# Performance work log

Hardware: AMD Instinct MI355X
Metric: run time of the kernel (lower is better)

## Reference

```python
import jax, jax.numpy as jnp
import numpy as np

B, S, E, U, V = 64, 1024, 1024, 1024, 32000

def setup_inputs() -> dict:
    key = jax.random.key(0)
    ks = jax.random.split(key, 12)
    s = lambda fan_in: 1.0 / np.sqrt(fan_in)
    return {
        "sentence": jax.random.randint(ks[0], (B, S), 0, V, dtype=jnp.int64),
        "emb": jax.random.normal(ks[1], (V, E), jnp.float32),
        "Wf": jax.random.normal(ks[2], (E, U), jnp.float32) * s(E),
        "bf": jnp.zeros((U,), jnp.float32),
        "Wi": jax.random.normal(ks[3], (E, U), jnp.float32) * s(E),
        "bi": jnp.zeros((U,), jnp.float32),
        "Wh": jax.random.normal(ks[4], (E, U), jnp.float32) * s(E),
        "bh": jnp.zeros((U,), jnp.float32),
        "W1": jax.random.normal(ks[5], (U, 64), jnp.float32) * s(U),
        "b1": jnp.zeros((64,), jnp.float32),
        "W2": jax.random.normal(ks[6], (64, 1), jnp.float32) * s(64),
        "b2": jnp.zeros((1,), jnp.float32),
    }

def reference(sentence, emb, Wf, bf, Wi, bi, Wh, bh, W1, b1, W2, b2):
    x = emb[sentence]                                   # [B,S,E]
    # minLSTM gates depend only on x -> hoist GEMMs out of the time loop
    f = jax.nn.sigmoid(jnp.einsum('bse,eu->bsu', x, Wf) + bf)
    i = jax.nn.sigmoid(jnp.einsum('bse,eu->bsu', x, Wi) + bi)
    h_tilde = jnp.einsum('bse,eu->bsu', x, Wh) + bh
    denom = f + i
    f_n = f / denom                                     # normalized forget gate
    i_n = i / denom                                     # normalized input gate

    def step(h, gates):
        f_t, ih_t = gates                               # [B,U] each
        h = f_t * h + ih_t
        return h, None

    h0 = jnp.zeros((sentence.shape[0], Wf.shape[1]), x.dtype)
    # scan over time; precombine i_n * h_tilde
    gates = (jnp.swapaxes(f_n, 0, 1), jnp.swapaxes(i_n * h_tilde, 0, 1))  # [S,B,U]
    h, _ = jax.lax.scan(step, h0, gates)
    z = h @ W1 + b1
    z = z @ W2 + b2
    return jax.nn.sigmoid(z)                            # [B,1]
```

## Files before the change

kernel.cpp:

```cpp
#include <hip/hip_runtime.h>
#include <cstdint>

typedef unsigned short u16;
typedef __attribute__((ext_vector_type(8))) short short8;
typedef __attribute__((ext_vector_type(8))) unsigned short ushort8;
typedef __attribute__((ext_vector_type(4))) float floatx4;
typedef __attribute__((ext_vector_type(8))) _Float16 half8;

#define S_LEN 1024
#define BATCH 64
#define EDIM 1024
#define UDIM 1024
#define VOCAB 32000
#define NTOT (3 * UDIM)
#define CT 64
#define NC (S_LEN / CT)
#define BUFE (128 * 64 + 192 * 64)

__device__ __forceinline__ u16 f2bf(float x) {
  unsigned u = __float_as_uint(x);
  return (u16)((u + 0x7fffu + ((u >> 16) & 1u)) >> 16);
}

__device__ __forceinline__ void async16(const u16* g, u16* s) {
  __builtin_amdgcn_global_load_lds(
      (__attribute__((address_space(1))) void*)(uintptr_t)g,
      (__attribute__((address_space(3))) void*)(uintptr_t)s,
      16, 0, 0);
}

__device__ __forceinline__ float sigm(float x) {
  return __builtin_amdgcn_rcpf(1.f + __expf(-x));
}

__global__ __launch_bounds__(256) void conv_emb(const float4* __restrict__ in,
                                                ushort4* __restrict__ out, int n4) {
  const int stride = gridDim.x * 256;
  for (int i = blockIdx.x * 256 + threadIdx.x; i < n4; i += stride) {
    float4 v = in[i];
    ushort4 o;
    o.x = f2bf(v.x); o.y = f2bf(v.y); o.z = f2bf(v.z); o.w = f2bf(v.w);
    out[i] = o;
  }
}

__global__ __launch_bounds__(256) void conv_wt(const float* __restrict__ Wf,
                                               const float* __restrict__ Wi,
                                               const float* __restrict__ Wh,
                                               u16* __restrict__ wtB) {
  __shared__ float t[32][33];
  const float* W = (blockIdx.z == 0) ? Wf : ((blockIdx.z == 1) ? Wi : Wh);
  int bx = blockIdx.x * 32;
  int by = blockIdx.y * 32;
  int tx = threadIdx.x, ty = threadIdx.y;
  for (int j = 0; j < 32; j += 8)
    t[ty + j][tx] = W[(size_t)(by + ty + j) * UDIM + bx + tx];
  __syncthreads();
  u16* out = wtB + (size_t)blockIdx.z * UDIM * EDIM;
  for (int j = 0; j < 32; j += 8)
    out[(size_t)(bx + ty + j) * EDIM + by + tx] = f2bf(t[tx][ty + j]);
}

__global__ __launch_bounds__(256, 2) void gate_gemm(
    const u16* __restrict__ embB, const u16* __restrict__ wtB,
    const float* __restrict__ bfp, const float* __restrict__ bip,
    const float* __restrict__ bhp, u16* __restrict__ FG) {
  __shared__ __align__(16) u16 SM[2 * BUFE];

  const int tid = threadIdx.x;
  const int wave = tid >> 6;
  const int lane = tid & 63;

  const int g = blockIdx.x;
  const int x = g & 7;
  const int s = g >> 3;
  const int mtile = s >> 1;
  const int utile = x * 2 + (s & 1);
  const int m0 = mtile * 128;
  const int u0 = utile * 64;

  const u16* gA[4]; int loA[4];
  const u16* gB[6]; int loB[6];
#pragma unroll
  for (int j = 0; j < 4; ++j) {
    int idx = j * 256 + tid;
    int r = idx >> 3;
    int cg = (idx & 7) ^ (r & 7);
    gA[j] = embB + (size_t)(m0 + r) * EDIM + cg * 8;
    loA[j] = idx * 8;
  }
#pragma unroll
  for (int j = 0; j < 6; ++j) {
    int idx = j * 256 + tid;
    int r = idx >> 3;
    int gr = (r >> 6) * UDIM + u0 + (r & 63);
    int cg = (idx & 7) ^ (r & 7);
    gB[j] = wtB + (size_t)gr * EDIM + cg * 8;
    loB[j] = 128 * 64 + idx * 8;
  }

  floatx4 acc[8][3] = {};
  const int fr = lane & 15;
  const int fq = lane >> 4;
  const int fr7 = fr & 7;
  const int un = wave * 16 + fr;

#pragma unroll
  for (int j = 0; j < 4; ++j) async16(gA[j], &SM[loA[j]]);
#pragma unroll
  for (int j = 0; j < 6; ++j) async16(gB[j], &SM[loB[j]]);
  asm volatile("s_waitcnt vmcnt(0)" ::: "memory");
  __builtin_amdgcn_s_barrier();
  __builtin_amdgcn_sched_barrier(0);

  int cur = 0;
  for (int t = 0; t < EDIM / 64; ++t) {
    if (t + 1 < EDIM / 64) {
      const int k0 = (t + 1) * 64;
      u16* nb = SM + (cur ^ 1) * BUFE;
#pragma unroll
      for (int j = 0; j < 4; ++j) async16(gA[j] + k0, &nb[loA[j]]);
#pragma unroll
      for (int j = 0; j < 6; ++j) async16(gB[j] + k0, &nb[loB[j]]);
    }
    __builtin_amdgcn_sched_barrier(0);
    const u16* As = SM + cur * BUFE;
    const u16* Bs = As + 128 * 64;
#pragma unroll
    for (int kk = 0; kk < 2; ++kk) {
      const int swz = ((kk * 4 + fq) ^ fr7) * 8;
      short8 b0 = *(const short8*)&Bs[(0 * 64 + un) * 64 + swz];
      short8 b1 = *(const short8*)&Bs[(1 * 64 + un) * 64 + swz];
      short8 b2 = *(const short8*)&Bs[(2 * 64 + un) * 64 + swz];
#pragma unroll
      for (int mt = 0; mt < 8; ++mt) {
        short8 am = *(const short8*)&As[(mt * 16 + fr) * 64 + swz];
        acc[mt][0] = __builtin_amdgcn_mfma_f32_16x16x32_bf16(am, b0, acc[mt][0], 0, 0, 0);
        acc[mt][1] = __builtin_amdgcn_mfma_f32_16x16x32_bf16(am, b1, acc[mt][1], 0, 0, 0);
        acc[mt][2] = __builtin_amdgcn_mfma_f32_16x16x32_bf16(am, b2, acc[mt][2], 0, 0, 0);
      }
    }
    __builtin_amdgcn_sched_barrier(0);
    asm volatile("s_waitcnt vmcnt(0)" ::: "memory");
    __builtin_amdgcn_s_barrier();
    __builtin_amdgcn_sched_barrier(0);
    cur ^= 1;
  }

  const int ug = u0 + un;
  const float bfv = bfp[ug], biv = bip[ug], bhv = bhp[ug];
  u16* FGs = SM;
  const int up = un ^ ((fq & 1) << 4);
#pragma unroll
  for (int mt = 0; mt < 8; ++mt) {
#pragma unroll
    for (int r = 0; r < 4; ++r) {
      float fs = sigm(acc[mt][0][r] + bfv);
      float is = sigm(acc[mt][1][r] + biv);
      float hv = acc[mt][2][r] + bhv;
      float inv = __builtin_amdgcn_rcpf(fs + is);
      float fn = fs * inv;
      float gv = is * inv * hv;
      int row = mt * 16 + fq * 4 + r;
      unsigned pkfg = (unsigned)__builtin_bit_cast(u16, (_Float16)fn) |
                      ((unsigned)__builtin_bit_cast(u16, (_Float16)gv) << 16);
      *(unsigned*)&FGs[row * 128 + up * 2] = pkfg;
    }
  }
  __syncthreads();
#pragma unroll
  for (int j = 0; j < 8; ++j) {
    int idx = j * 256 + tid;
    int row = idx >> 4, cc = idx & 15;
    int ccp = cc ^ (((row >> 2) & 1) << 2);
    *(ushort8*)&FG[(size_t)(m0 + row) * (2 * UDIM) + u0 * 2 + cc * 8] =
        *(const ushort8*)&FGs[row * 128 + ccp * 8];
  }
}

__global__ __launch_bounds__(256) void scan_gather(
    const int* __restrict__ sent, const u16* __restrict__ FG,
    float* __restrict__ Fc, float* __restrict__ Gc) {
  const int b = blockIdx.x >> 4;
  const int c = blockIdx.x & (NC - 1);
  const int tid = threadIdx.x;
  __shared__ int toks[CT];
  if (tid < CT) toks[tid] = sent[b * S_LEN + c * CT + tid];
  __syncthreads();
  const int uo2 = tid * 8;
  floatx4 F = {1.f, 1.f, 1.f, 1.f};
  floatx4 G = {0.f, 0.f, 0.f, 0.f};
#pragma unroll 8
  for (int t = 0; t < CT; ++t) {
    const size_t ro = (size_t)toks[t] * (2 * UDIM) + uo2;
    half8 fg = __builtin_bit_cast(half8, *(const ushort8*)&FG[ro]);
    floatx4 fn = {(float)fg[0], (float)fg[2], (float)fg[4], (float)fg[6]};
    floatx4 gv = {(float)fg[1], (float)fg[3], (float)fg[5], (float)fg[7]};
    G = fn * G + gv;
    F = F * fn;
  }
  const size_t o = (size_t)c * (BATCH * UDIM) + (size_t)b * UDIM + tid * 4;
  *(floatx4*)&Fc[o] = F;
  *(floatx4*)&Gc[o] = G;
}

__global__ __launch_bounds__(256) void mlp_head(
    const float* __restrict__ Fc, const float* __restrict__ Gc,
    const float* __restrict__ W1, const float* __restrict__ b1,
    const float* __restrict__ W2, const float* __restrict__ b2,
    float* __restrict__ out) {
  const int b = blockIdx.x;
  const int tid = threadIdx.x;
  __shared__ float h_s[UDIM];
  __shared__ float z1[64];
  for (int u = tid; u < UDIM; u += 256) {
    float h = 0.f;
#pragma unroll
    for (int c = 0; c < NC; ++c) {
      float F = Fc[c * (BATCH * UDIM) + b * UDIM + u];
      float G = Gc[c * (BATCH * UDIM) + b * UDIM + u];
      h = F * h + G;
    }
    h_s[u] = h;
  }
  __syncthreads();
  const int j = tid >> 2, p = tid & 3;
  float partial = 0.f;
  for (int u = p * 256; u < p * 256 + 256; ++u) partial += h_s[u] * W1[u * 64 + j];
  partial += __shfl_down(partial, 1);
  partial += __shfl_down(partial, 2);
  if (p == 0) z1[j] = partial + b1[j];
  __syncthreads();
  if (tid < 64) {
    float v = z1[tid] * W2[tid];
#pragma unroll
    for (int off = 32; off > 0; off >>= 1) v += __shfl_down(v, off);
    if (tid == 0) out[b] = 1.f / (1.f + __expf(-(v + b2[0])));
  }
}

extern "C" void kernel_launch(void* const* d_in, const int* in_sizes, int n_in,
                              void* d_out, int out_size, void* d_ws, size_t ws_size,
                              hipStream_t stream) {
  const int* sent = (const int*)d_in[0];
  const float* emb = (const float*)d_in[1];
  const float* Wf = (const float*)d_in[2];
  const float* bf_ = (const float*)d_in[3];
  const float* Wi = (const float*)d_in[4];
  const float* bi_ = (const float*)d_in[5];
  const float* Wh = (const float*)d_in[6];
  const float* bh_ = (const float*)d_in[7];
  const float* W1 = (const float*)d_in[8];
  const float* b1 = (const float*)d_in[9];
  const float* W2 = (const float*)d_in[10];
  const float* b2 = (const float*)d_in[11];
  float* out = (float*)d_out;

  char* ws = (char*)d_ws;
  u16* embB = (u16*)ws;   ws += (size_t)VOCAB * EDIM * 2;
  u16* wtB = (u16*)ws;    ws += (size_t)NTOT * EDIM * 2;
  u16* FG = (u16*)ws;     ws += (size_t)VOCAB * UDIM * 2 * 2;
  float* Fc = (float*)ws; ws += (size_t)NC * BATCH * UDIM * 4;
  float* Gc = (float*)ws; ws += (size_t)NC * BATCH * UDIM * 4;

  int n4 = (int)((size_t)VOCAB * EDIM / 4);
  hipLaunchKernelGGL(conv_emb, dim3(2048), dim3(256), 0, stream,
                     (const float4*)emb, (ushort4*)embB, n4);
  hipLaunchKernelGGL(conv_wt, dim3(32, 32, 3), dim3(32, 8), 0, stream, Wf, Wi, Wh, wtB);
  hipLaunchKernelGGL(gate_gemm, dim3((VOCAB / 128) * (NTOT / 192)), dim3(256), 0, stream,
                     embB, wtB, bf_, bi_, bh_, FG);
  hipLaunchKernelGGL(scan_gather, dim3(BATCH * NC), dim3(256), 0, stream,
                     sent, FG, Fc, Gc);
  hipLaunchKernelGGL(mlp_head, dim3(BATCH), dim3(256), 0, stream, Fc, Gc, W1, b1, W2, b2, out);
}
```

Before: 468.9 us.

## Restructure gate GEMM into finer-grained K-slice pipeline with higher occupancy

After: 477.5 us. No clear change (+1.8%).

```diff
diff --git a/kernel.cpp b/kernel.cpp
--- a/kernel.cpp
+++ b/kernel.cpp
@@ -15,7 +15,9 @@
 #define NTOT (3 * UDIM)
 #define CT 64
 #define NC (S_LEN / CT)
-#define BUFE (128 * 64 + 192 * 64)
+#define A_HALF 4096
+#define B_BASE 8192
+#define B_HALF 6144
 
 __device__ __forceinline__ u16 f2bf(float x) {
   unsigned u = __float_as_uint(x);
@@ -36,7 +38,17 @@
 __global__ __launch_bounds__(256) void conv_emb(const float4* __restrict__ in,
                                                 ushort4* __restrict__ out, int n4) {
   const int stride = gridDim.x * 256;
-  for (int i = blockIdx.x * 256 + threadIdx.x; i < n4; i += stride) {
+  int i = blockIdx.x * 256 + threadIdx.x;
+  for (; i + stride < n4; i += 2 * stride) {
+    float4 v0 = in[i];
+    float4 v1 = in[i + stride];
+    ushort4 o0, o1;
+    o0.x = f2bf(v0.x); o0.y = f2bf(v0.y); o0.z = f2bf(v0.z); o0.w = f2bf(v0.w);
+    o1.x = f2bf(v1.x); o1.y = f2bf(v1.y); o1.z = f2bf(v1.z); o1.w = f2bf(v1.w);
+    out[i] = o0;
+    out[i + stride] = o1;
+  }
+  if (i < n4) {
     float4 v = in[i];
     ushort4 o;
     o.x = f2bf(v.x); o.y = f2bf(v.y); o.z = f2bf(v.z); o.w = f2bf(v.w);
@@ -61,11 +73,11 @@
     out[(size_t)(bx + ty + j) * EDIM + by + tx] = f2bf(t[tx][ty + j]);
 }
 
-__global__ __launch_bounds__(256, 2) void gate_gemm(
+__global__ __launch_bounds__(256, 3) void gate_gemm(
     const u16* __restrict__ embB, const u16* __restrict__ wtB,
     const float* __restrict__ bfp, const float* __restrict__ bip,
     const float* __restrict__ bhp, u16* __restrict__ FG) {
-  __shared__ __align__(16) u16 SM[2 * BUFE];
+  __shared__ __align__(16) u16 SM[2 * A_HALF + 2 * B_HALF];
 
   const int tid = threadIdx.x;
   const int wave = tid >> 6;
@@ -79,73 +91,93 @@
   const int m0 = mtile * 128;
   const int u0 = utile * 64;
 
-  const u16* gA[4]; int loA[4];
-  const u16* gB[6]; int loB[6];
-#pragma unroll
-  for (int j = 0; j < 4; ++j) {
+  const u16* gA[2]; int loA[2];
+  const u16* gB[3]; int loB[3];
+#pragma unroll
+  for (int j = 0; j < 2; ++j) {
     int idx = j * 256 + tid;
-    int r = idx >> 3;
-    int cg = (idx & 7) ^ (r & 7);
-    gA[j] = embB + (size_t)(m0 + r) * EDIM + cg * 8;
+    int r = idx >> 2;
+    int sub = (idx & 3) ^ ((r >> 1) & 3);
+    gA[j] = embB + (size_t)(m0 + r) * EDIM + sub * 8;
     loA[j] = idx * 8;
   }
 #pragma unroll
-  for (int j = 0; j < 6; ++j) {
+  for (int j = 0; j < 3; ++j) {
     int idx = j * 256 + tid;
-    int r = idx >> 3;
+    int r = idx >> 2;
     int gr = (r >> 6) * UDIM + u0 + (r & 63);
-    int cg = (idx & 7) ^ (r & 7);
-    gB[j] = wtB + (size_t)gr * EDIM + cg * 8;
-    loB[j] = 128 * 64 + idx * 8;
+    int sub = (idx & 3) ^ ((r >> 1) & 3);
+    gB[j] = wtB + (size_t)gr * EDIM + sub * 8;
+    loB[j] = idx * 8;
   }
 
   floatx4 acc[8][3] = {};
   const int fr = lane & 15;
   const int fq = lane >> 4;
-  const int fr7 = fr & 7;
   const int un = wave * 16 + fr;
-
-#pragma unroll
-  for (int j = 0; j < 4; ++j) async16(gA[j], &SM[loA[j]]);
-#pragma unroll
-  for (int j = 0; j < 6; ++j) async16(gB[j], &SM[loB[j]]);
+  const int crd = (fq ^ ((fr >> 1) & 3)) * 8;
+
+#define STAGE(p, h)                                                  \
+  do {                                                               \
+    const int kb_ = (p) * 32;                                        \
+    _Pragma("unroll") for (int j = 0; j < 2; ++j)                    \
+        async16(gA[j] + kb_, &SM[(h) * A_HALF + loA[j]]);            \
+    _Pragma("unroll") for (int j = 0; j < 3; ++j)                    \
+        async16(gB[j] + kb_, &SM[B_BASE + (h) * B_HALF + loB[j]]);   \
+  } while (0)
+
+#define COMPUTE(h)                                                   \
+  do {                                                               \
+    const u16* Ah = SM + (h) * A_HALF;                               \
+    const u16* Bh = SM + B_BASE + (h) * B_HALF;                      \
+    short8 b0 = *(const short8*)&Bh[(0 * 64 + un) * 32 + crd];       \
+    short8 b1 = *(const short8*)&Bh[(1 * 64 + un) * 32 + crd];       \
+    short8 b2 = *(const short8*)&Bh[(2 * 64 + un) * 32 + crd];       \
+    __builtin_amdgcn_s_setprio(1);                                   \
+    _Pragma("unroll") for (int mt = 0; mt < 8; ++mt) {               \
+      short8 am = *(const short8*)&Ah[(mt * 16 + fr) * 32 + crd];    \
+      acc[mt][0] = __builtin_amdgcn_mfma_f32_16x16x32_bf16(am, b0, acc[mt][0], 0, 0, 0); \
+      acc[mt][1] = __builtin_amdgcn_mfma_f32_16x16x32_bf16(am, b1, acc[mt][1], 0, 0, 0); \
+      acc[mt][2] = __builtin_amdgcn_mfma_f32_16x16x32_bf16(am, b2, acc[mt][2], 0, 0, 0); \
+    }                                                                \
+    __builtin_amdgcn_s_setprio(0);                                   \
+  } while (0)
+
+  STAGE(0, 0);
+  STAGE(1, 1);
+  __builtin_amdgcn_sched_barrier(0);
+
+  for (int t = 0; t < 15; ++t) {
+    asm volatile("s_waitcnt vmcnt(5)" ::: "memory");
+    __builtin_amdgcn_s_barrier();
+    __builtin_amdgcn_sched_barrier(0);
+    COMPUTE(0);
+    __builtin_amdgcn_sched_barrier(0);
+    __builtin_amdgcn_s_barrier();
+    STAGE(2 * t + 2, 0);
+    __builtin_amdgcn_sched_barrier(0);
+    asm volatile("s_waitcnt vmcnt(5)" ::: "memory");
+    __builtin_amdgcn_s_barrier();
+    __builtin_amdgcn_sched_barrier(0);
+    COMPUTE(1);
+    __builtin_amdgcn_sched_barrier(0);
+    __builtin_amdgcn_s_barrier();
+    STAGE(2 * t + 3, 1);
+    __builtin_amdgcn_sched_barrier(0);
+  }
+  asm volatile("s_waitcnt vmcnt(5)" ::: "memory");
+  __builtin_amdgcn_s_barrier();
+  __builtin_amdgcn_sched_barrier(0);
+  COMPUTE(0);
+  __builtin_amdgcn_sched_barrier(0);
+  __builtin_amdgcn_s_barrier();
   asm volatile("s_waitcnt vmcnt(0)" ::: "memory");
   __builtin_amdgcn_s_barrier();
   __builtin_amdgcn_sched_barrier(0);
-
-  int cur = 0;
-  for (int t = 0; t < EDIM / 64; ++t) {
-    if (t + 1 < EDIM / 64) {
-      const int k0 = (t + 1) * 64;
-      u16* nb = SM + (cur ^ 1) * BUFE;
-#pragma unroll
-      for (int j = 0; j < 4; ++j) async16(gA[j] + k0, &nb[loA[j]]);
-#pragma unroll
-      for (int j = 0; j < 6; ++j) async16(gB[j] + k0, &nb[loB[j]]);
-    }
-    __builtin_amdgcn_sched_barrier(0);
-    const u16* As = SM + cur * BUFE;
-    const u16* Bs = As + 128 * 64;
-#pragma unroll
-    for (int kk = 0; kk < 2; ++kk) {
-      const int swz = ((kk * 4 + fq) ^ fr7) * 8;
-      short8 b0 = *(const short8*)&Bs[(0 * 64 + un) * 64 + swz];
-      short8 b1 = *(const short8*)&Bs[(1 * 64 + un) * 64 + swz];
-      short8 b2 = *(const short8*)&Bs[(2 * 64 + un) * 64 + swz];
-#pragma unroll
-      for (int mt = 0; mt < 8; ++mt) {
-        short8 am = *(const short8*)&As[(mt * 16 + fr) * 64 + swz];
-        acc[mt][0] = __builtin_amdgcn_mfma_f32_16x16x32_bf16(am, b0, acc[mt][0], 0, 0, 0);
-        acc[mt][1] = __builtin_amdgcn_mfma_f32_16x16x32_bf16(am, b1, acc[mt][1], 0, 0, 0);
-        acc[mt][2] = __builtin_amdgcn_mfma_f32_16x16x32_bf16(am, b2, acc[mt][2], 0, 0, 0);
-      }
-    }
-    __builtin_amdgcn_sched_barrier(0);
-    asm volatile("s_waitcnt vmcnt(0)" ::: "memory");
-    __builtin_amdgcn_s_barrier();
-    __builtin_amdgcn_sched_barrier(0);
-    cur ^= 1;
-  }
+  COMPUTE(1);
+  __syncthreads();
+#undef STAGE
+#undef COMPUTE
 
   const int ug = u0 + un;
   const float bfv = bfp[ug], biv = bip[ug], bhv = bhp[ug];
```
